# Kernel tuning notes

Hardware: AMD Instinct MI355X
Metric: run time of the kernel (lower is better)

## Reference

```python
import jax, jax.numpy as jnp
import numpy as np

NT, NS, NH, NG = 365, 1024, 64, 32
NW = NH * 8 + 2


def setup_inputs() -> dict:
    key = jax.random.key(0)
    k1, k2, k3, k4 = jax.random.split(key, 4)
    std = 1.0 / np.sqrt(NH)
    x = jax.random.normal(k1, (NT, NS, 4), dtype=jnp.float32)
    # make P (precip) nonnegative and T1 < T2 plausible-ish; math is still generic
    xc = jax.random.normal(k2, (NS, NG), dtype=jnp.float32)
    fc_w = jax.random.uniform(k3, (NW, NG), minval=-std, maxval=std, dtype=jnp.float32)
    fc_b = jax.random.uniform(k4, (NW,), minval=-std, maxval=std, dtype=jnp.float32)
    return {"x": x, "xc": xc, "fc_w": fc_w, "fc_b": fc_b}


def reference(x, xc, fc_w, fc_b):
    nh = NH
    P, E, T1, T2 = x[..., 0], x[..., 1], x[..., 2], x[..., 3]  # each [nt, ns]
    Ta = (T1 + T2) * 0.5
    # rain/snow partition: rP = 1 - arccos((T1+T2)/(T2-T1))/3.1415, masked
    valid = (T1 < 0) & (T2 > 0)
    denom = jnp.where(valid, T2 - T1, 1.0)
    ratio = jnp.clip(jnp.where(valid, (T1 + T2) / denom, 0.0), -0.999999, 0.999999)
    rP = 1.0 - jnp.arccos(ratio) / 3.1415
    rP = jnp.where(T1 >= 0, 1.0, rP)
    rP = jnp.where(T2 <= 0, 0.0, rP)
    Ps = (1.0 - rP) * P  # snow   [nt, ns]
    Pl = rP * P          # liquid [nt, ns]

    w = xc @ fc_w.T + fc_b  # [ns, nh*8+2]
    gm = jnp.exp(w[:, :nh]) + 1.0
    ge = jax.nn.sigmoid(w[:, nh:2 * nh]) * 2.0
    go = jax.nn.sigmoid(w[:, 2 * nh:3 * nh])
    gl = jnp.exp(w[:, 3 * nh:4 * nh] * 2.0)
    ga = jax.nn.softmax(w[:, 4 * nh:5 * nh], axis=1)  # Dropout in eval mode = identity
    gb = jax.nn.sigmoid(w[:, 5 * nh:6 * nh])
    qb = jax.nn.relu(w[:, -1]) / nh  # [ns]
    kb = jax.nn.sigmoid(w[:, 6 * nh:7 * nh]) / 10.0
    gi = jax.nn.sigmoid(w[:, 7 * nh:8 * nh])

    ns = P.shape[1]
    init = (jnp.zeros((ns, nh), jnp.float32),) * 3  # S0, H0, G0

    def step(carry, inp):
        S0, H0, G0 = carry
        Ps_k, Pl_k, Ta_k, E_k = inp  # each [ns]
        S = S0 + Ps_k[:, None]
        Sm = jnp.minimum(S0, jax.nn.relu(Ta_k[:, None] * gm))  # snowmelt
        H = jax.nn.relu(H0 + Sm + Pl_k[:, None] * gi - E_k[:, None] * ge)
        Q1 = jax.nn.relu(H - gl)
        Q2a = jnp.minimum(H, gl) * go
        Q2 = Q2a * (1.0 - gb)
        G = G0 + Q2a * gb
        Q3 = G * kb
        H0n = jnp.minimum(H - Q2a, gl)
        G0n = G - Q3
        S0n = S - Sm
        Y = jnp.sum((Q1 + Q2 + Q3 + qb[:, None]) * ga, axis=1)  # [ns]
        return (S0n, H0n, G0n), Y

    _, Yout = jax.lax.scan(step, init, (Ps, Pl, Ta, E))
    return Yout  # [nt, ns]
```

## Files before the change

kernel.cpp:

```cpp
#include <hip/hip_runtime.h>
#include <math.h>

#define NT_ 365
#define NS_ 1024
#define NH_ 64
#define NG_ 32
#define NW_ 514
#define CH_ 64
#define NCHUNK_ 6
#define YPAD_ 65
#define SUB_ 8

__device__ __forceinline__ float sigmoidf(float v) {
  return 1.0f / (1.0f + expf(-v));
}

__device__ __forceinline__ float4 compute_met(float4 xv) {
  const float P = xv.x, E = xv.y, T1 = xv.z, T2 = xv.w;
  const float Ta = (T1 + T2) * 0.5f;
  float rP;
  if (T2 <= 0.0f) {
    rP = 0.0f;
  } else if (T1 >= 0.0f) {
    rP = 1.0f;
  } else {
    float r = (T1 + T2) / (T2 - T1);
    r = fminf(fmaxf(r, -0.999999f), 0.999999f);
    rP = 1.0f - acosf(r) * (1.0f / 3.1415f);
  }
  float4 m;
  m.x = (1.0f - rP) * P;
  m.y = rP * P;
  m.z = fmaxf(Ta, 0.0f);
  m.w = E;
  return m;
}

__global__ __launch_bounds__(256) void waternet_scan(
    const float* __restrict__ x,
    const float* __restrict__ xc,
    const float* __restrict__ fc_w,
    const float* __restrict__ fc_b,
    float* __restrict__ out)
{
  __shared__ float4 smet[4][CH_];
  __shared__ float  ytile[4][CH_ * YPAD_];

  const int tid  = threadIdx.x;
  const int lane = tid & 63;
  const int wv   = tid >> 6;
  const int site = (blockIdx.x << 2) + wv;
  const int us   = __builtin_amdgcn_readfirstlane(site);
  const float4* xp = (const float4*)x;

  float4 xcur = xp[lane * NS_ + site];

  float acc[8];
#pragma unroll
  for (int k = 0; k < 8; ++k) acc[k] = fc_b[k * NH_ + lane];
  float accq = fc_b[NW_ - 1];

  const float4* xcq = (const float4*)(xc + us * NG_);
  const float4* wq4 = (const float4*)fc_w;
#pragma unroll
  for (int g4 = 0; g4 < NG_ / 4; ++g4) {
    const float4 xv = xcq[g4];
#pragma unroll
    for (int k = 0; k < 8; ++k) {
      const float4 w = wq4[(k * NH_ + lane) * (NG_ / 4) + g4];
      acc[k] = fmaf(xv.x, w.x, acc[k]);
      acc[k] = fmaf(xv.y, w.y, acc[k]);
      acc[k] = fmaf(xv.z, w.z, acc[k]);
      acc[k] = fmaf(xv.w, w.w, acc[k]);
    }
    {
      const float4 w = wq4[(NW_ - 1) * (NG_ / 4) + g4];
      accq = fmaf(xv.x, w.x, accq);
      accq = fmaf(xv.y, w.y, accq);
      accq = fmaf(xv.z, w.z, accq);
      accq = fmaf(xv.w, w.w, accq);
    }
  }

  const float gm = expf(acc[0]) + 1.0f;
  const float ge = sigmoidf(acc[1]) * 2.0f;
  const float go = sigmoidf(acc[2]);
  const float gl = expf(acc[3] * 2.0f);
  float mx = acc[4];
#pragma unroll
  for (int mm = 32; mm >= 1; mm >>= 1) mx = fmaxf(mx, __shfl_xor(mx, mm, 64));
  const float ex = expf(acc[4] - mx);
  float sm = ex;
#pragma unroll
  for (int mm = 32; mm >= 1; mm >>= 1) sm += __shfl_xor(sm, mm, 64);
  const float ga = ex / sm;
  const float gb = sigmoidf(acc[5]);
  const float kb = sigmoidf(acc[6]) * 0.1f;
  const float gi = sigmoidf(acc[7]);
  const float qb = fmaxf(accq, 0.0f) * (1.0f / NH_);
  const float kb1m = 1.0f - kb;
  const float nge  = -ge;
  const float gq1  = go * (1.0f - gb) - 1.0f;

  float S0 = 0.0f, H0 = 0.0f, G0 = 0.0f;

  smet[wv][lane] = compute_met(xcur);

  auto step = [&](const float4 mt, float* ywaddr) {
    const float melt = mt.z * gm;
    const float Sm   = fminf(S0, melt);
    const float base = H0 + Sm;
    S0 = (S0 - Sm) + mt.x;
    const float t3 = fmaf(mt.y, gi, base);
    const float H  = fmaxf(fmaf(mt.w, nge, t3), 0.0f);
    const float M  = fminf(H, gl);
    const float Q2a = M * go;
    H0 = fminf(H - Q2a, gl);
    const float G = fmaf(Q2a, gb, G0);
    G0 = G * kb1m;
    *ywaddr = fmaf(G, kb, fmaf(M, gq1, H)) * ga;
  };

  float*       yw = &ytile[wv][lane];
  const float* yr = &ytile[wv][lane * YPAD_];

#pragma unroll 1
  for (int c = 0; c < NCHUNK_; ++c) {
    int tn = (c + 1) * CH_ + lane;
    tn = (tn < NT_) ? tn : (NT_ - 1);
    const float4 xnext = xp[tn * NS_ + site];

    const float4* mp = &smet[wv][0];

    float4 mb0[SUB_], mb1[SUB_];
#pragma unroll
    for (int u = 0; u < SUB_; ++u) mb0[u] = mp[u];

#pragma unroll
    for (int sc = 0; sc < CH_ / SUB_; ++sc) {
      float4*       cur = (sc & 1) ? mb1 : mb0;
      float4*       nxt = (sc & 1) ? mb0 : mb1;
      if (sc < CH_ / SUB_ - 1) {
#pragma unroll
        for (int u = 0; u < SUB_; ++u) nxt[u] = mp[SUB_ * (sc + 1) + u];
      }
#pragma unroll
      for (int u = 0; u < SUB_; ++u)
        step(cur[u], yw + (SUB_ * sc + u) * YPAD_);
    }

    float r0 = 0.0f, r1 = 0.0f, r2 = 0.0f, r3 = 0.0f;
#pragma unroll
    for (int h = 0; h < CH_; h += 4) {
      r0 += yr[h + 0];
      r1 += yr[h + 1];
      r2 += yr[h + 2];
      r3 += yr[h + 3];
    }
    const int t_out = c * CH_ + lane;
    if (t_out < NT_) out[t_out * NS_ + site] = ((r0 + r1) + (r2 + r3)) + qb;

    if (c + 1 < NCHUNK_) smet[wv][lane] = compute_met(xnext);
  }
}

extern "C" void kernel_launch(void* const* d_in, const int* in_sizes, int n_in,
                              void* d_out, int out_size, void* d_ws, size_t ws_size,
                              hipStream_t stream) {
  const float* x    = (const float*)d_in[0];
  const float* xc   = (const float*)d_in[1];
  const float* fc_w = (const float*)d_in[2];
  const float* fc_b = (const float*)d_in[3];
  float* out = (float*)d_out;

  hipLaunchKernelGGL(waternet_scan, dim3(NS_ / 4), dim3(256), 0, stream,
                     x, xc, fc_w, fc_b, out);
}
```

Baseline: 87.52 us.

## Split scan into snow-producer and soil-consumer waves pipelined through shared memory

The recurrence is split into two parts. A snow wave computes the snow state S and the per-step input d. It takes the forcing data through readlane broadcasts and writes d into a double-buffered shared-memory array. A second wave per site consumes d to run the H/G recurrence and the output reduction. The block grows to 512 threads and the dense projection is split between the two wave groups. The aim is to shorten the serial per-step dependency chain by overlapping the two halves across waves, at the cost of a block-wide barrier every 32 steps and extra shared memory.

Measured after the change: 93.34 us. +6.7%, slower.

```diff
diff --git a/kernel.cpp b/kernel.cpp
--- a/kernel.cpp
+++ b/kernel.cpp
@@ -7,12 +7,15 @@
 #define NG_ 32
 #define NW_ 514
 #define CH_ 64
-#define NCHUNK_ 6
+#define PH_ 32
 #define YPAD_ 65
-#define SUB_ 8
 
 __device__ __forceinline__ float sigmoidf(float v) {
   return 1.0f / (1.0f + expf(-v));
+}
+
+__device__ __forceinline__ float rdl(float v, int l) {
+  return __int_as_float(__builtin_amdgcn_readlane(__float_as_int(v), l));
 }
 
 __device__ __forceinline__ float4 compute_met(float4 xv) {
@@ -36,132 +39,190 @@
   return m;
 }
 
-__global__ __launch_bounds__(256) void waternet_scan(
+__global__ __launch_bounds__(512) void waternet_scan(
     const float* __restrict__ x,
     const float* __restrict__ xc,
     const float* __restrict__ fc_w,
     const float* __restrict__ fc_b,
     float* __restrict__ out)
 {
-  __shared__ float4 smet[4][CH_];
-  __shared__ float  ytile[4][CH_ * YPAD_];
+  __shared__ float dsm[2][4][PH_][NH_];
+  __shared__ float ytile[4][CH_ * YPAD_];
 
   const int tid  = threadIdx.x;
   const int lane = tid & 63;
   const int wv   = tid >> 6;
-  const int site = (blockIdx.x << 2) + wv;
+  const int myv  = wv & 3;
+  const bool isS = (wv >= 4);
+  const int site = (blockIdx.x << 2) + myv;
   const int us   = __builtin_amdgcn_readfirstlane(site);
-  const float4* xp = (const float4*)x;
-
-  float4 xcur = xp[lane * NS_ + site];
-
-  float acc[8];
-#pragma unroll
-  for (int k = 0; k < 8; ++k) acc[k] = fc_b[k * NH_ + lane];
-  float accq = fc_b[NW_ - 1];
-
+  const float4* xp  = (const float4*)x;
   const float4* xcq = (const float4*)(xc + us * NG_);
   const float4* wq4 = (const float4*)fc_w;
-#pragma unroll
-  for (int g4 = 0; g4 < NG_ / 4; ++g4) {
-    const float4 xv = xcq[g4];
-#pragma unroll
-    for (int k = 0; k < 8; ++k) {
-      const float4 w = wq4[(k * NH_ + lane) * (NG_ / 4) + g4];
-      acc[k] = fmaf(xv.x, w.x, acc[k]);
-      acc[k] = fmaf(xv.y, w.y, acc[k]);
-      acc[k] = fmaf(xv.z, w.z, acc[k]);
-      acc[k] = fmaf(xv.w, w.w, acc[k]);
-    }
-    {
-      const float4 w = wq4[(NW_ - 1) * (NG_ / 4) + g4];
-      accq = fmaf(xv.x, w.x, accq);
-      accq = fmaf(xv.y, w.y, accq);
-      accq = fmaf(xv.z, w.z, accq);
-      accq = fmaf(xv.w, w.w, accq);
-    }
+
+  float gm = 0.f, nge = 0.f, gi = 0.f;
+  float gl = 0.f, mgo = 0.f, kb1m = 0.f, gbgo = 0.f;
+  float ga = 0.f, c1 = 0.f, c2 = 0.f, qb = 0.f;
+  float4 mm    = make_float4(0.f, 0.f, 0.f, 0.f);
+  float4 xnext = make_float4(0.f, 0.f, 0.f, 0.f);
+  float S0 = 0.f, H0 = 0.f, G = 0.f;
+
+  if (isS) {
+    const float4 xcur = xp[lane * NS_ + site];
+    xnext = xp[(CH_ + lane) * NS_ + site];
+    float a0 = fc_b[0 * NH_ + lane];
+    float a1 = fc_b[1 * NH_ + lane];
+    float a7 = fc_b[7 * NH_ + lane];
+#pragma unroll
+    for (int g4 = 0; g4 < NG_ / 4; ++g4) {
+      const float4 xv = xcq[g4];
+      const float4 w0 = wq4[(0 * NH_ + lane) * (NG_ / 4) + g4];
+      const float4 w1 = wq4[(1 * NH_ + lane) * (NG_ / 4) + g4];
+      const float4 w7 = wq4[(7 * NH_ + lane) * (NG_ / 4) + g4];
+      a0 = fmaf(xv.x, w0.x, a0); a0 = fmaf(xv.y, w0.y, a0);
+      a0 = fmaf(xv.z, w0.z, a0); a0 = fmaf(xv.w, w0.w, a0);
+      a1 = fmaf(xv.x, w1.x, a1); a1 = fmaf(xv.y, w1.y, a1);
+      a1 = fmaf(xv.z, w1.z, a1); a1 = fmaf(xv.w, w1.w, a1);
+      a7 = fmaf(xv.x, w7.x, a7); a7 = fmaf(xv.y, w7.y, a7);
+      a7 = fmaf(xv.z, w7.z, a7); a7 = fmaf(xv.w, w7.w, a7);
+    }
+    gm  = expf(a0) + 1.0f;
+    nge = -2.0f * sigmoidf(a1);
+    gi  = sigmoidf(a7);
+    mm  = compute_met(xcur);
+  } else {
+    float a2 = fc_b[2 * NH_ + lane];
+    float a3 = fc_b[3 * NH_ + lane];
+    float a4 = fc_b[4 * NH_ + lane];
+    float a5 = fc_b[5 * NH_ + lane];
+    float a6 = fc_b[6 * NH_ + lane];
+    float aq = fc_b[NW_ - 1];
+#pragma unroll
+    for (int g4 = 0; g4 < NG_ / 4; ++g4) {
+      const float4 xv = xcq[g4];
+      const float4 w2 = wq4[(2 * NH_ + lane) * (NG_ / 4) + g4];
+      const float4 w3 = wq4[(3 * NH_ + lane) * (NG_ / 4) + g4];
+      const float4 w4 = wq4[(4 * NH_ + lane) * (NG_ / 4) + g4];
+      const float4 w5 = wq4[(5 * NH_ + lane) * (NG_ / 4) + g4];
+      const float4 w6 = wq4[(6 * NH_ + lane) * (NG_ / 4) + g4];
+      const float4 wq = wq4[(NW_ - 1) * (NG_ / 4) + g4];
+      a2 = fmaf(xv.x, w2.x, a2); a2 = fmaf(xv.y, w2.y, a2);
+      a2 = fmaf(xv.z, w2.z, a2); a2 = fmaf(xv.w, w2.w, a2);
+      a3 = fmaf(xv.x, w3.x, a3); a3 = fmaf(xv.y, w3.y, a3);
+      a3 = fmaf(xv.z, w3.z, a3); a3 = fmaf(xv.w, w3.w, a3);
+      a4 = fmaf(xv.x, w4.x, a4); a4 = fmaf(xv.y, w4.y, a4);
+      a4 = fmaf(xv.z, w4.z, a4); a4 = fmaf(xv.w, w4.w, a4);
+      a5 = fmaf(xv.x, w5.x, a5); a5 = fmaf(xv.y, w5.y, a5);
+      a5 = fmaf(xv.z, w5.z, a5); a5 = fmaf(xv.w, w5.w, a5);
+      a6 = fmaf(xv.x, w6.x, a6); a6 = fmaf(xv.y, w6.y, a6);
+      a6 = fmaf(xv.z, w6.z, a6); a6 = fmaf(xv.w, w6.w, a6);
+      aq = fmaf(xv.x, wq.x, aq); aq = fmaf(xv.y, wq.y, aq);
+      aq = fmaf(xv.z, wq.z, aq); aq = fmaf(xv.w, wq.w, aq);
+    }
+    const float go = sigmoidf(a2);
+    gl = expf(a3 * 2.0f);
+    float mx = a4;
+#pragma unroll
+    for (int sh = 32; sh >= 1; sh >>= 1) mx = fmaxf(mx, __shfl_xor(mx, sh, 64));
+    const float ex = expf(a4 - mx);
+    float sme = ex;
+#pragma unroll
+    for (int sh = 32; sh >= 1; sh >>= 1) sme += __shfl_xor(sme, sh, 64);
+    ga = ex / sme;
+    const float gb = sigmoidf(a5);
+    const float kb = sigmoidf(a6) * 0.1f;
+    qb   = fmaxf(aq, 0.0f) * (1.0f / NH_);
+    mgo  = -go;
+    kb1m = 1.0f - kb;
+    gbgo = gb * go;
+    c1 = ga * (go * (1.0f - gb) - 1.0f);
+    c2 = ga * kb;
   }
 
-  const float gm = expf(acc[0]) + 1.0f;
-  const float ge = sigmoidf(acc[1]) * 2.0f;
-  const float go = sigmoidf(acc[2]);
-  const float gl = expf(acc[3] * 2.0f);
-  float mx = acc[4];
-#pragma unroll
-  for (int mm = 32; mm >= 1; mm >>= 1) mx = fmaxf(mx, __shfl_xor(mx, mm, 64));
-  const float ex = expf(acc[4] - mx);
-  float sm = ex;
-#pragma unroll
-  for (int mm = 32; mm >= 1; mm >>= 1) sm += __shfl_xor(sm, mm, 64);
-  const float ga = ex / sm;
-  const float gb = sigmoidf(acc[5]);
-  const float kb = sigmoidf(acc[6]) * 0.1f;
-  const float gi = sigmoidf(acc[7]);
-  const float qb = fmaxf(accq, 0.0f) * (1.0f / NH_);
-  const float kb1m = 1.0f - kb;
-  const float nge  = -ge;
-  const float gq1  = go * (1.0f - gb) - 1.0f;
-
-  float S0 = 0.0f, H0 = 0.0f, G0 = 0.0f;
-
-  smet[wv][lane] = compute_met(xcur);
-
-  auto step = [&](const float4 mt, float* ywaddr) {
-    const float melt = mt.z * gm;
-    const float Sm   = fminf(S0, melt);
-    const float base = H0 + Sm;
-    S0 = (S0 - Sm) + mt.x;
-    const float t3 = fmaf(mt.y, gi, base);
-    const float H  = fmaxf(fmaf(mt.w, nge, t3), 0.0f);
-    const float M  = fminf(H, gl);
-    const float Q2a = M * go;
-    H0 = fminf(H - Q2a, gl);
-    const float G = fmaf(Q2a, gb, G0);
-    G0 = G * kb1m;
-    *ywaddr = fmaf(G, kb, fmaf(M, gq1, H)) * ga;
-  };
-
-  float*       yw = &ytile[wv][lane];
-  const float* yr = &ytile[wv][lane * YPAD_];
-
-#pragma unroll 1
-  for (int c = 0; c < NCHUNK_; ++c) {
-    int tn = (c + 1) * CH_ + lane;
-    tn = (tn < NT_) ? tn : (NT_ - 1);
-    const float4 xnext = xp[tn * NS_ + site];
-
-    const float4* mp = &smet[wv][0];
-
-    float4 mb0[SUB_], mb1[SUB_];
-#pragma unroll
-    for (int u = 0; u < SUB_; ++u) mb0[u] = mp[u];
-
-#pragma unroll
-    for (int sc = 0; sc < CH_ / SUB_; ++sc) {
-      float4*       cur = (sc & 1) ? mb1 : mb0;
-      float4*       nxt = (sc & 1) ? mb0 : mb1;
-      if (sc < CH_ / SUB_ - 1) {
-#pragma unroll
-        for (int u = 0; u < SUB_; ++u) nxt[u] = mp[SUB_ * (sc + 1) + u];
-      }
-#pragma unroll
-      for (int u = 0; u < SUB_; ++u)
-        step(cur[u], yw + (SUB_ * sc + u) * YPAD_);
-    }
-
-    float r0 = 0.0f, r1 = 0.0f, r2 = 0.0f, r3 = 0.0f;
-#pragma unroll
-    for (int h = 0; h < CH_; h += 4) {
-      r0 += yr[h + 0];
-      r1 += yr[h + 1];
-      r2 += yr[h + 2];
-      r3 += yr[h + 3];
+  auto produce = [&](int ph) {
+    float* ob = &dsm[ph & 1][myv][0][lane];
+    const int tb = (ph & 1) << 5;
+#pragma unroll
+    for (int u = 0; u < PH_; ++u) {
+      const float Ps = rdl(mm.x, tb + u);
+      const float Pl = rdl(mm.y, tb + u);
+      const float Tz = rdl(mm.z, tb + u);
+      const float Ev = rdl(mm.w, tb + u);
+      const float melt = Tz * gm;
+      const float dd = S0 - melt;
+      const float r  = fmaxf(dd, 0.0f);
+      const float Sm = S0 - r;
+      const float d  = fmaf(Pl, gi, fmaf(Ev, nge, Sm));
+      S0 = r + Ps;
+      ob[u * NH_] = d;
+    }
+  };
+
+  auto hstep = [&](float d, float* ywaddr) {
+    const float z  = H0 + d;
+    const float Hh = fmaxf(z, 0.0f);
+    const float M  = __builtin_amdgcn_fmed3f(z, 0.0f, gl);
+    H0 = fminf(fmaf(mgo, M, Hh), gl);
+    G  = fmaf(kb1m, G, gbgo * M);
+    *ywaddr = fmaf(c2, G, fmaf(c1, M, ga * Hh));
+  };
+
+  auto consume = [&](int ph) {
+    const float* db = &dsm[ph & 1][myv][0][lane];
+    float* ywp = &ytile[myv][lane + (((ph & 1) << 5) * YPAD_)];
+    float dA[8], dB[8];
+#pragma unroll
+    for (int i = 0; i < 8; ++i) dA[i] = db[i * NH_];
+#pragma unroll
+    for (int i = 0; i < 8; ++i) dB[i] = db[(8 + i) * NH_];
+#pragma unroll
+    for (int u = 0; u < 8; ++u) hstep(dA[u], ywp + u * YPAD_);
+#pragma unroll
+    for (int i = 0; i < 8; ++i) dA[i] = db[(16 + i) * NH_];
+#pragma unroll
+    for (int u = 0; u < 8; ++u) hstep(dB[u], ywp + (8 + u) * YPAD_);
+#pragma unroll
+    for (int i = 0; i < 8; ++i) dB[i] = db[(24 + i) * NH_];
+#pragma unroll
+    for (int u = 0; u < 8; ++u) hstep(dA[u], ywp + (16 + u) * YPAD_);
+#pragma unroll
+    for (int u = 0; u < 8; ++u) hstep(dB[u], ywp + (24 + u) * YPAD_);
+  };
+
+  auto reduce_out = [&](int c) {
+    const float* yrr = &ytile[myv][lane * YPAD_];
+    float r0 = 0.f, r1 = 0.f, r2 = 0.f, r3 = 0.f;
+#pragma unroll
+    for (int h2 = 0; h2 < CH_; h2 += 4) {
+      r0 += yrr[h2 + 0];
+      r1 += yrr[h2 + 1];
+      r2 += yrr[h2 + 2];
+      r3 += yrr[h2 + 3];
     }
     const int t_out = c * CH_ + lane;
     if (t_out < NT_) out[t_out * NS_ + site] = ((r0 + r1) + (r2 + r3)) + qb;
-
-    if (c + 1 < NCHUNK_) smet[wv][lane] = compute_met(xnext);
+  };
+
+  if (isS) produce(0);
+  __syncthreads();
+
+#pragma unroll 1
+  for (int s = 1; s < 12; ++s) {
+    if (isS) {
+      produce(s);
+      if ((s & 1) && s < 11) {
+        mm = compute_met(xnext);
+        int t2 = ((s >> 1) + 2) * CH_ + lane;
+        if (t2 > NT_ - 1) t2 = NT_ - 1;
+        xnext = xp[t2 * NS_ + site];
+      }
+    } else {
+      consume(s - 1);
+      if ((s - 1) & 1) reduce_out((s - 1) >> 1);
+    }
+    __syncthreads();
   }
+  if (!isS) { consume(11); reduce_out(5); }
 }
 
 extern "C" void kernel_launch(void* const* d_in, const int* in_sizes, int n_in,
@@ -173,6 +234,6 @@
   const float* fc_b = (const float*)d_in[3];
   float* out = (float*)d_out;
 
-  hipLaunchKernelGGL(waternet_scan, dim3(NS_ / 4), dim3(256), 0, stream,
+  hipLaunchKernelGGL(waternet_scan, dim3(NS_ / 4), dim3(512), 0, stream,
                      x, xc, fc_w, fc_b, out);
 }
```

## Interleave two sites per wavefront and simplify the recurrence step

Applied to the files above, without the earlier changes.

Each wavefront now runs the scan for two independent sites, interleaving their steps so the serial dependency chains overlap and give the scheduler independent work. Blocks shrink to 128 threads with the same grid. The step is rewritten algebraically: med3 for clamping, folded gate constants with ga premultiplied, and fewer dependent ops on the critical path. This halves wavefront count and thus occupancy, and raises register use.

Measured after the change: 99.73 us. +14.0%, slower.

```diff
diff --git a/kernel.cpp b/kernel.cpp
--- a/kernel.cpp
+++ b/kernel.cpp
@@ -9,7 +9,7 @@
 #define CH_ 64
 #define NCHUNK_ 6
 #define YPAD_ 65
-#define SUB_ 8
+#define SUB_ 4
 
 __device__ __forceinline__ float sigmoidf(float v) {
   return 1.0f / (1.0f + expf(-v));
@@ -36,7 +36,13 @@
   return m;
 }
 
-__global__ __launch_bounds__(256) void waternet_scan(
+struct Gates {
+  float gm, nge, gi;
+  float gl, mgo, kb1m, gbgo;
+  float ga, c1, c2, qb;
+};
+
+__global__ __launch_bounds__(128) void waternet_scan(
     const float* __restrict__ x,
     const float* __restrict__ xc,
     const float* __restrict__ fc_w,
@@ -49,118 +55,152 @@
   const int tid  = threadIdx.x;
   const int lane = tid & 63;
   const int wv   = tid >> 6;
-  const int site = (blockIdx.x << 2) + wv;
-  const int us   = __builtin_amdgcn_readfirstlane(site);
-  const float4* xp = (const float4*)x;
-
-  float4 xcur = xp[lane * NS_ + site];
-
-  float acc[8];
-#pragma unroll
-  for (int k = 0; k < 8; ++k) acc[k] = fc_b[k * NH_ + lane];
-  float accq = fc_b[NW_ - 1];
-
-  const float4* xcq = (const float4*)(xc + us * NG_);
+  const int ssA  = wv * 2, ssB = ssA + 1;
+  const int siteA = (blockIdx.x << 2) + ssA;
+  const int siteB = siteA + 1;
+  const int uA = __builtin_amdgcn_readfirstlane(siteA);
+  const float4* xp  = (const float4*)x;
   const float4* wq4 = (const float4*)fc_w;
+
+  float4 xcA = xp[lane * NS_ + siteA];
+  float4 xcB = xp[lane * NS_ + siteB];
+
+  float aA[8], aB[8];
+#pragma unroll
+  for (int k = 0; k < 8; ++k) { aA[k] = fc_b[k * NH_ + lane]; aB[k] = aA[k]; }
+  float aqA = fc_b[NW_ - 1], aqB = aqA;
+
+  const float4* xcqA = (const float4*)(xc + uA * NG_);
+  const float4* xcqB = (const float4*)(xc + (uA + 1) * NG_);
 #pragma unroll
   for (int g4 = 0; g4 < NG_ / 4; ++g4) {
-    const float4 xv = xcq[g4];
+    const float4 xA = xcqA[g4];
+    const float4 xB = xcqB[g4];
 #pragma unroll
     for (int k = 0; k < 8; ++k) {
       const float4 w = wq4[(k * NH_ + lane) * (NG_ / 4) + g4];
-      acc[k] = fmaf(xv.x, w.x, acc[k]);
-      acc[k] = fmaf(xv.y, w.y, acc[k]);
-      acc[k] = fmaf(xv.z, w.z, acc[k]);
-      acc[k] = fmaf(xv.w, w.w, acc[k]);
+      aA[k] = fmaf(xA.x, w.x, aA[k]); aA[k] = fmaf(xA.y, w.y, aA[k]);
+      aA[k] = fmaf(xA.z, w.z, aA[k]); aA[k] = fmaf(xA.w, w.w, aA[k]);
+      aB[k] = fmaf(xB.x, w.x, aB[k]); aB[k] = fmaf(xB.y, w.y, aB[k]);
+      aB[k] = fmaf(xB.z, w.z, aB[k]); aB[k] = fmaf(xB.w, w.w, aB[k]);
     }
     {
       const float4 w = wq4[(NW_ - 1) * (NG_ / 4) + g4];
-      accq = fmaf(xv.x, w.x, accq);
-      accq = fmaf(xv.y, w.y, accq);
-      accq = fmaf(xv.z, w.z, accq);
-      accq = fmaf(xv.w, w.w, accq);
+      aqA = fmaf(xA.x, w.x, aqA); aqA = fmaf(xA.y, w.y, aqA);
+      aqA = fmaf(xA.z, w.z, aqA); aqA = fmaf(xA.w, w.w, aqA);
+      aqB = fmaf(xB.x, w.x, aqB); aqB = fmaf(xB.y, w.y, aqB);
+      aqB = fmaf(xB.z, w.z, aqB); aqB = fmaf(xB.w, w.w, aqB);
     }
   }
 
-  const float gm = expf(acc[0]) + 1.0f;
-  const float ge = sigmoidf(acc[1]) * 2.0f;
-  const float go = sigmoidf(acc[2]);
-  const float gl = expf(acc[3] * 2.0f);
-  float mx = acc[4];
-#pragma unroll
-  for (int mm = 32; mm >= 1; mm >>= 1) mx = fmaxf(mx, __shfl_xor(mx, mm, 64));
-  const float ex = expf(acc[4] - mx);
-  float sm = ex;
-#pragma unroll
-  for (int mm = 32; mm >= 1; mm >>= 1) sm += __shfl_xor(sm, mm, 64);
-  const float ga = ex / sm;
-  const float gb = sigmoidf(acc[5]);
-  const float kb = sigmoidf(acc[6]) * 0.1f;
-  const float gi = sigmoidf(acc[7]);
-  const float qb = fmaxf(accq, 0.0f) * (1.0f / NH_);
-  const float kb1m = 1.0f - kb;
-  const float nge  = -ge;
-  const float gq1  = go * (1.0f - gb) - 1.0f;
-
-  float S0 = 0.0f, H0 = 0.0f, G0 = 0.0f;
-
-  smet[wv][lane] = compute_met(xcur);
-
-  auto step = [&](const float4 mt, float* ywaddr) {
-    const float melt = mt.z * gm;
-    const float Sm   = fminf(S0, melt);
-    const float base = H0 + Sm;
-    S0 = (S0 - Sm) + mt.x;
-    const float t3 = fmaf(mt.y, gi, base);
-    const float H  = fmaxf(fmaf(mt.w, nge, t3), 0.0f);
-    const float M  = fminf(H, gl);
-    const float Q2a = M * go;
-    H0 = fminf(H - Q2a, gl);
-    const float G = fmaf(Q2a, gb, G0);
-    G0 = G * kb1m;
-    *ywaddr = fmaf(G, kb, fmaf(M, gq1, H)) * ga;
+  auto mkgates = [&](const float a[8], float aq) -> Gates {
+    Gates g;
+    g.gm  = expf(a[0]) + 1.0f;
+    g.nge = -2.0f * sigmoidf(a[1]);
+    const float go = sigmoidf(a[2]);
+    g.gl  = expf(a[3] * 2.0f);
+    float mx = a[4];
+#pragma unroll
+    for (int mm = 32; mm >= 1; mm >>= 1) mx = fmaxf(mx, __shfl_xor(mx, mm, 64));
+    const float ex = expf(a[4] - mx);
+    float sm = ex;
+#pragma unroll
+    for (int mm = 32; mm >= 1; mm >>= 1) sm += __shfl_xor(sm, mm, 64);
+    g.ga = ex / sm;
+    const float gb = sigmoidf(a[5]);
+    const float kb = sigmoidf(a[6]) * 0.1f;
+    g.gi   = sigmoidf(a[7]);
+    g.qb   = fmaxf(aq, 0.0f) * (1.0f / NH_);
+    g.mgo  = -go;
+    g.kb1m = 1.0f - kb;
+    g.gbgo = gb * go;
+    g.c1 = g.ga * (go * (1.0f - gb) - 1.0f);
+    g.c2 = g.ga * kb;
+    return g;
   };
-
-  float*       yw = &ytile[wv][lane];
-  const float* yr = &ytile[wv][lane * YPAD_];
+  const Gates gA = mkgates(aA, aqA);
+  const Gates gB = mkgates(aB, aqB);
+
+  float S0A = 0.f, H0A = 0.f, GA = 0.f;
+  float S0B = 0.f, H0B = 0.f, GB = 0.f;
+
+  smet[ssA][lane] = compute_met(xcA);
+  smet[ssB][lane] = compute_met(xcB);
+
+  auto pstep = [&](const Gates& g, float& S0, float& H0, float& G,
+                   const float4 m, float* ywaddr) {
+    const float melt = m.z * g.gm;
+    const float r    = fmaxf(S0 - melt, 0.0f);
+    const float Sm   = S0 - r;
+    const float d    = fmaf(m.y, g.gi, fmaf(m.w, g.nge, Sm));
+    S0 = r + m.x;
+    const float z  = H0 + d;
+    const float Hh = fmaxf(z, 0.0f);
+    const float M  = __builtin_amdgcn_fmed3f(z, 0.0f, g.gl);
+    H0 = fminf(fmaf(g.mgo, M, Hh), g.gl);
+    G  = fmaf(g.kb1m, G, g.gbgo * M);
+    *ywaddr = fmaf(g.c2, G, fmaf(g.c1, M, g.ga * Hh));
+  };
+
+  float*       ywA = &ytile[ssA][lane];
+  float*       ywB = &ytile[ssB][lane];
+  const float* yrA = &ytile[ssA][lane * YPAD_];
+  const float* yrB = &ytile[ssB][lane * YPAD_];
 
 #pragma unroll 1
   for (int c = 0; c < NCHUNK_; ++c) {
     int tn = (c + 1) * CH_ + lane;
     tn = (tn < NT_) ? tn : (NT_ - 1);
-    const float4 xnext = xp[tn * NS_ + site];
-
-    const float4* mp = &smet[wv][0];
-
-    float4 mb0[SUB_], mb1[SUB_];
-#pragma unroll
-    for (int u = 0; u < SUB_; ++u) mb0[u] = mp[u];
+    const float4 xnA = xp[tn * NS_ + siteA];
+    const float4 xnB = xp[tn * NS_ + siteB];
+
+    const float4* mpA = &smet[ssA][0];
+    const float4* mpB = &smet[ssB][0];
+
+    float4 mA0[SUB_], mA1[SUB_], mB0[SUB_], mB1[SUB_];
+#pragma unroll
+    for (int u = 0; u < SUB_; ++u) { mA0[u] = mpA[u]; mB0[u] = mpB[u]; }
 
 #pragma unroll
     for (int sc = 0; sc < CH_ / SUB_; ++sc) {
-      float4*       cur = (sc & 1) ? mb1 : mb0;
-      float4*       nxt = (sc & 1) ? mb0 : mb1;
+      float4* cA = (sc & 1) ? mA1 : mA0;
+      float4* nA = (sc & 1) ? mA0 : mA1;
+      float4* cB = (sc & 1) ? mB1 : mB0;
+      float4* nB = (sc & 1) ? mB0 : mB1;
       if (sc < CH_ / SUB_ - 1) {
 #pragma unroll
-        for (int u = 0; u < SUB_; ++u) nxt[u] = mp[SUB_ * (sc + 1) + u];
+        for (int u = 0; u < SUB_; ++u) {
+          nA[u] = mpA[SUB_ * (sc + 1) + u];
+          nB[u] = mpB[SUB_ * (sc + 1) + u];
+        }
       }
 #pragma unroll
-      for (int u = 0; u < SUB_; ++u)
-        step(cur[u], yw + (SUB_ * sc + u) * YPAD_);
-    }
-
-    float r0 = 0.0f, r1 = 0.0f, r2 = 0.0f, r3 = 0.0f;
+      for (int u = 0; u < SUB_; ++u) {
+        const int j = SUB_ * sc + u;
+        pstep(gA, S0A, H0A, GA, cA[u], ywA + j * YPAD_);
+        pstep(gB, S0B, H0B, GB, cB[u], ywB + j * YPAD_);
+      }
+    }
+
+    float rA0 = 0.f, rA1 = 0.f, rA2 = 0.f, rA3 = 0.f;
+    float rB0 = 0.f, rB1 = 0.f, rB2 = 0.f, rB3 = 0.f;
 #pragma unroll
     for (int h = 0; h < CH_; h += 4) {
-      r0 += yr[h + 0];
-      r1 += yr[h + 1];
-      r2 += yr[h + 2];
-      r3 += yr[h + 3];
+      rA0 += yrA[h + 0]; rA1 += yrA[h + 1];
+      rA2 += yrA[h + 2]; rA3 += yrA[h + 3];
+      rB0 += yrB[h + 0]; rB1 += yrB[h + 1];
+      rB2 += yrB[h + 2]; rB3 += yrB[h + 3];
     }
     const int t_out = c * CH_ + lane;
-    if (t_out < NT_) out[t_out * NS_ + site] = ((r0 + r1) + (r2 + r3)) + qb;
-
-    if (c + 1 < NCHUNK_) smet[wv][lane] = compute_met(xnext);
+    if (t_out < NT_) {
+      out[t_out * NS_ + siteA] = ((rA0 + rA1) + (rA2 + rA3)) + gA.qb;
+      out[t_out * NS_ + siteB] = ((rB0 + rB1) + (rB2 + rB3)) + gB.qb;
+    }
+
+    if (c + 1 < NCHUNK_) {
+      smet[ssA][lane] = compute_met(xnA);
+      smet[ssB][lane] = compute_met(xnB);
+    }
   }
 }
 
@@ -173,6 +213,6 @@
   const float* fc_b = (const float*)d_in[3];
   float* out = (float*)d_out;
 
-  hipLaunchKernelGGL(waternet_scan, dim3(NS_ / 4), dim3(256), 0, stream,
+  hipLaunchKernelGGL(waternet_scan, dim3(NS_ / 4), dim3(128), 0, stream,
                      x, xc, fc_w, fc_b, out);
 }
```

## Broadcast per-step inputs via readlane and restructure scan recurrence algebra

Applied to the files above, without the earlier changes.

Removes the shared-memory staging of per-timestep meteorological inputs. Each step now broadcasts the current timestep's values from the owning lane with readlane into scalar registers, instead of double-buffered LDS loads. The recurrence is also rewritten algebraically: the snowmelt min becomes a relu subtraction, H and M share a med3, the G update is fused as G*(1-kb)+gb*go*M, and the ga scaling is folded into the coefficients. The aim is to cut LDS traffic and ALU ops on the serial dependency chain. It relies on the compiler emitting efficient readlane-to-SGPR moves, and small floating-point reassociation differences are possible.

After: 88.59 us. About the same (+1.2%).

```diff
diff --git a/kernel.cpp b/kernel.cpp
--- a/kernel.cpp
+++ b/kernel.cpp
@@ -9,10 +9,13 @@
 #define CH_ 64
 #define NCHUNK_ 6
 #define YPAD_ 65
-#define SUB_ 8
 
 __device__ __forceinline__ float sigmoidf(float v) {
   return 1.0f / (1.0f + expf(-v));
+}
+
+__device__ __forceinline__ float rdl(float v, int l) {
+  return __int_as_float(__builtin_amdgcn_readlane(__float_as_int(v), l));
 }
 
 __device__ __forceinline__ float4 compute_met(float4 xv) {
@@ -43,8 +46,7 @@
     const float* __restrict__ fc_b,
     float* __restrict__ out)
 {
-  __shared__ float4 smet[4][CH_];
-  __shared__ float  ytile[4][CH_ * YPAD_];
+  __shared__ float ytile[4][CH_ * YPAD_];
 
   const int tid  = threadIdx.x;
   const int lane = tid & 63;
@@ -83,43 +85,30 @@
   }
 
   const float gm = expf(acc[0]) + 1.0f;
-  const float ge = sigmoidf(acc[1]) * 2.0f;
+  const float nge = -2.0f * sigmoidf(acc[1]);
   const float go = sigmoidf(acc[2]);
   const float gl = expf(acc[3] * 2.0f);
   float mx = acc[4];
 #pragma unroll
-  for (int mm = 32; mm >= 1; mm >>= 1) mx = fmaxf(mx, __shfl_xor(mx, mm, 64));
+  for (int mm2 = 32; mm2 >= 1; mm2 >>= 1) mx = fmaxf(mx, __shfl_xor(mx, mm2, 64));
   const float ex = expf(acc[4] - mx);
   float sm = ex;
 #pragma unroll
-  for (int mm = 32; mm >= 1; mm >>= 1) sm += __shfl_xor(sm, mm, 64);
+  for (int mm2 = 32; mm2 >= 1; mm2 >>= 1) sm += __shfl_xor(sm, mm2, 64);
   const float ga = ex / sm;
   const float gb = sigmoidf(acc[5]);
   const float kb = sigmoidf(acc[6]) * 0.1f;
   const float gi = sigmoidf(acc[7]);
   const float qb = fmaxf(accq, 0.0f) * (1.0f / NH_);
+  const float mgo  = -go;
   const float kb1m = 1.0f - kb;
-  const float nge  = -ge;
-  const float gq1  = go * (1.0f - gb) - 1.0f;
+  const float gbgo = gb * go;
+  const float c1 = ga * (go * (1.0f - gb) - 1.0f);
+  const float c2 = ga * kb;
 
-  float S0 = 0.0f, H0 = 0.0f, G0 = 0.0f;
+  float S0 = 0.0f, H0 = 0.0f, G = 0.0f;
 
-  smet[wv][lane] = compute_met(xcur);
-
-  auto step = [&](const float4 mt, float* ywaddr) {
-    const float melt = mt.z * gm;
-    const float Sm   = fminf(S0, melt);
-    const float base = H0 + Sm;
-    S0 = (S0 - Sm) + mt.x;
-    const float t3 = fmaf(mt.y, gi, base);
-    const float H  = fmaxf(fmaf(mt.w, nge, t3), 0.0f);
-    const float M  = fminf(H, gl);
-    const float Q2a = M * go;
-    H0 = fminf(H - Q2a, gl);
-    const float G = fmaf(Q2a, gb, G0);
-    G0 = G * kb1m;
-    *ywaddr = fmaf(G, kb, fmaf(M, gq1, H)) * ga;
-  };
+  float4 mm = compute_met(xcur);
 
   float*       yw = &ytile[wv][lane];
   const float* yr = &ytile[wv][lane * YPAD_];
@@ -130,23 +119,23 @@
     tn = (tn < NT_) ? tn : (NT_ - 1);
     const float4 xnext = xp[tn * NS_ + site];
 
-    const float4* mp = &smet[wv][0];
-
-    float4 mb0[SUB_], mb1[SUB_];
 #pragma unroll
-    for (int u = 0; u < SUB_; ++u) mb0[u] = mp[u];
-
-#pragma unroll
-    for (int sc = 0; sc < CH_ / SUB_; ++sc) {
-      float4*       cur = (sc & 1) ? mb1 : mb0;
-      float4*       nxt = (sc & 1) ? mb0 : mb1;
-      if (sc < CH_ / SUB_ - 1) {
-#pragma unroll
-        for (int u = 0; u < SUB_; ++u) nxt[u] = mp[SUB_ * (sc + 1) + u];
-      }
-#pragma unroll
-      for (int u = 0; u < SUB_; ++u)
-        step(cur[u], yw + (SUB_ * sc + u) * YPAD_);
+    for (int u = 0; u < CH_; ++u) {
+      const float Ps = rdl(mm.x, u);
+      const float Pl = rdl(mm.y, u);
+      const float Tz = rdl(mm.z, u);
+      const float Ev = rdl(mm.w, u);
+      const float melt = Tz * gm;
+      const float r    = fmaxf(S0 - melt, 0.0f);
+      const float Sm   = S0 - r;
+      const float d    = fmaf(Pl, gi, fmaf(Ev, nge, Sm));
+      S0 = r + Ps;
+      const float z  = H0 + d;
+      const float Hh = fmaxf(z, 0.0f);
+      const float M  = __builtin_amdgcn_fmed3f(z, 0.0f, gl);
+      H0 = fminf(fmaf(mgo, M, Hh), gl);
+      G  = fmaf(kb1m, G, gbgo * M);
+      yw[u * YPAD_] = fmaf(c2, G, fmaf(c1, M, ga * Hh));
     }
 
     float r0 = 0.0f, r1 = 0.0f, r2 = 0.0f, r3 = 0.0f;
@@ -160,7 +149,7 @@
     const int t_out = c * CH_ + lane;
     if (t_out < NT_) out[t_out * NS_ + site] = ((r0 + r1) + (r2 + r3)) + qb;
 
-    if (c + 1 < NCHUNK_) smet[wv][lane] = compute_met(xnext);
+    mm = compute_met(xnext);
   }
 }
 
```
